# Kernel tuning notes

Measured on AMD Instinct MI355X. Metric: run time of the kernel, lower is better.

The kernel has to match this reference:

```python
import jax, jax.numpy as jnp
import numpy as np

BN_EPS = 1e-5


def setup_inputs() -> dict:
    key = jax.random.key(0)
    ks = jax.random.split(key, 8)
    B, C_IN, C_OUT, N, K = 4, 32, 64, 32768, 16
    feature = jax.random.normal(ks[0], (B, C_IN, N), dtype=jnp.float32)
    knn_inds = jax.random.randint(ks[1], (B, N, K), 0, N, dtype=jnp.int64)
    W1 = jax.random.normal(ks[2], (C_OUT, C_IN), dtype=jnp.float32) * 0.05
    W2 = jax.random.normal(ks[3], (C_OUT, C_IN), dtype=jnp.float32) * 0.05
    bn_gamma = jax.random.uniform(ks[4], (2 * C_OUT,), dtype=jnp.float32) + 0.5
    bn_beta = jax.random.normal(ks[5], (2 * C_OUT,), dtype=jnp.float32) * 0.1
    bn_mean = jax.random.normal(ks[6], (2 * C_OUT,), dtype=jnp.float32) * 0.1
    bn_var = jax.random.uniform(ks[7], (2 * C_OUT,), dtype=jnp.float32) + 0.5
    return {"feature": feature, "knn_inds": knn_inds, "W1": W1, "W2": W2,
            "bn_gamma": bn_gamma, "bn_beta": bn_beta, "bn_mean": bn_mean, "bn_var": bn_var}


def reference(feature, knn_inds, W1, W2, bn_gamma, bn_beta, bn_mean, bn_var):
    B, C_in, N = feature.shape
    K = knn_inds.shape[2]
    # 1x1 Conv1d == per-point GEMM
    local = jnp.einsum('oc,bcn->bon', W1, feature)   # (B, C_out, N)
    edge = jnp.einsum('oc,bcn->bon', W2, feature)    # (B, C_out, N)
    C = local.shape[1]
    # KNN gather: neighbour[b,c,n,j] = edge[b,c,knn_inds[b,n,j]]
    idx = knn_inds.reshape(B, 1, N * K)              # broadcast over channel dim
    neighbour = jnp.take_along_axis(edge, idx, axis=2).reshape(B, C, N, K)
    central = local[:, :, :, None]                   # (B, C, N, 1)
    diff = neighbour - central
    ef = jnp.concatenate([jnp.broadcast_to(central, (B, C, N, K)), diff], axis=1)  # (B, 2C, N, K)
    # BatchNorm2d (eval mode: running stats) + ReLU
    inv = (bn_gamma / jnp.sqrt(bn_var + BN_EPS)).reshape(1, 2 * C, 1, 1)
    shift = (bn_beta - bn_mean * bn_gamma / jnp.sqrt(bn_var + BN_EPS)).reshape(1, 2 * C, 1, 1)
    ef = jax.nn.relu(ef * inv + shift)
    return jnp.mean(ef, axis=3)                      # (B, 2C, N)
```

## Files before the change

### kernel.cpp

```cpp
#include <hip/hip_runtime.h>
#include <hip/hip_fp16.h>

#define CIN 32
#define COUT 64
#define NB 4
#define NPTS 32768
#define KNN 16

typedef unsigned short u16;
typedef unsigned char u8;
typedef float f2v __attribute__((ext_vector_type(2)));

__device__ __forceinline__ u16 f2h(float f) {
  _Float16 h = (_Float16)f;
  u16 u; __builtin_memcpy(&u, &h, 2); return u;
}
__device__ __forceinline__ f2v h2_to_f2(unsigned int u) {
  _Float16 a, b;
  __builtin_memcpy(&a, (const char*)&u, 2);
  __builtin_memcpy(&b, ((const char*)&u) + 2, 2);
  return (f2v){(float)a, (float)b};
}

__global__ __launch_bounds__(256) void k1_gemm(
    const float* __restrict__ feat, const float* __restrict__ W1,
    const float* __restrict__ W2, const float* __restrict__ gamma,
    const float* __restrict__ beta, const float* __restrict__ mean,
    const float* __restrict__ var, u16* __restrict__ lt, u8* __restrict__ et,
    float* __restrict__ out) {
  const int bid = blockIdx.x;
  const int b = bid >> 9;
  const int n0 = (bid & 511) << 6;
  const int t = threadIdx.x;
  const int lane = t & 63;
  const int wchunk = __builtin_amdgcn_readfirstlane(t >> 6);
  const int n = n0 + lane;

  f2v fv[16];
  const float* fp = feat + (size_t)b * CIN * NPTS + n;
#pragma unroll
  for (int c2 = 0; c2 < 16; ++c2)
    fv[c2] = (f2v){fp[(size_t)(2 * c2) * NPTS], fp[(size_t)(2 * c2 + 1) * NPTS]};

  const int half = wchunk >> 1;
  const int rbase = (wchunk & 1) * 32;
  const float* Wp = half ? W2 : W1;

  unsigned int pkh[16];
  unsigned int pk8[8];

#pragma unroll
  for (int oo = 0; oo < 32; oo += 4) {
    const float* w0 = Wp + (size_t)(rbase + oo) * CIN;
    const f2v* wr0 = reinterpret_cast<const f2v*>(w0);
    const f2v* wr1 = reinterpret_cast<const f2v*>(w0 + CIN);
    const f2v* wr2 = reinterpret_cast<const f2v*>(w0 + 2 * CIN);
    const f2v* wr3 = reinterpret_cast<const f2v*>(w0 + 3 * CIN);
    f2v p0 = (f2v)0.f, p1 = (f2v)0.f, p2 = (f2v)0.f, p3 = (f2v)0.f;
#pragma unroll
    for (int c2 = 0; c2 < 16; ++c2) {
      const f2v fc = fv[c2];
      p0 = __builtin_elementwise_fma(wr0[c2], fc, p0);
      p1 = __builtin_elementwise_fma(wr1[c2], fc, p1);
      p2 = __builtin_elementwise_fma(wr2[c2], fc, p2);
      p3 = __builtin_elementwise_fma(wr3[c2], fc, p3);
    }
    const float a0 = p0.x + p0.y, a1 = p1.x + p1.y;
    const float a2 = p2.x + p2.y, a3 = p3.x + p3.y;
    if (half == 0) {
      pkh[oo / 2]     = (unsigned)f2h(a0) | ((unsigned)f2h(a1) << 16);
      pkh[oo / 2 + 1] = (unsigned)f2h(a2) | ((unsigned)f2h(a3) << 16);
      const float acc[4] = {a0, a1, a2, a3};
#pragma unroll
      for (int i = 0; i < 4; ++i) {
        const int r = rbase + oo + i;
        const float iv = gamma[r] * rsqrtf(var[r] + 1e-5f);
        const float sh = beta[r] - mean[r] * iv;
        out[((size_t)b * 128 + r) * NPTS + n] = fmaxf(fmaf(acc[i], iv, sh), 0.f);
      }
    } else {
      int u = 0;
      u = __builtin_amdgcn_cvt_pk_fp8_f32(a0, a1, u, false);
      u = __builtin_amdgcn_cvt_pk_fp8_f32(a2, a3, u, true);
      pk8[oo / 4] = (unsigned)u;
    }
  }
  if (half == 0) {
    uint4* dp = reinterpret_cast<uint4*>(lt + ((size_t)(b * NPTS + n)) * COUT + rbase);
#pragma unroll
    for (int q = 0; q < 4; ++q)
      dp[q] = make_uint4(pkh[4 * q], pkh[4 * q + 1], pkh[4 * q + 2], pkh[4 * q + 3]);
  } else {
    uint4* dp = reinterpret_cast<uint4*>(et + ((size_t)(b * NPTS + n)) * COUT + rbase);
    dp[0] = make_uint4(pk8[0], pk8[1], pk8[2], pk8[3]);
    dp[1] = make_uint4(pk8[4], pk8[5], pk8[6], pk8[7]);
  }
}

__global__ __launch_bounds__(256) void k2_gather(
    const u16* __restrict__ lt, const u8* __restrict__ et,
    const int* __restrict__ knn, const float* __restrict__ gamma,
    const float* __restrict__ beta, const float* __restrict__ mean,
    const float* __restrict__ var, float* __restrict__ out) {
  __shared__ float obuf[64 * 33];
  int bid = blockIdx.x;
  bid = (bid & 7) * 512 + (bid >> 3);
  const int b = bid >> 10;
  const int n_blk = (bid & 1023) << 5;
  const int t = threadIdx.x;
  const int w = t >> 6;
  const int lane = t & 63;
  const int nn = lane >> 3;
  const int cg = lane & 7;
  const int ch = cg * 8;

  f2v inv[4], sh[4];
#pragma unroll
  for (int i = 0; i < 4; ++i) {
    const int r0 = 64 + ch + 2 * i;
    const float iv0 = gamma[r0] * rsqrtf(var[r0] + 1e-5f);
    const float iv1 = gamma[r0 + 1] * rsqrtf(var[r0 + 1] + 1e-5f);
    inv[i] = (f2v){iv0, iv1};
    sh[i] = (f2v){beta[r0] - mean[r0] * iv0, beta[r0 + 1] - mean[r0 + 1] * iv1};
  }

  const int n = n_blk + w * 8 + nn;
  const size_t rowbase = (size_t)b * NPTS;

  const int4* kp = reinterpret_cast<const int4*>(knn + (rowbase + n) * KNN);
  const int4 kv0 = kp[0], kv1 = kp[1], kv2 = kp[2], kv3 = kp[3];
  const uint4 lv = *reinterpret_cast<const uint4*>(lt + (rowbase + n) * COUT + ch);

  const u8* etb = et + rowbase * COUT + ch;
  uint2 e[16];
  const int idx[16] = {kv0.x, kv0.y, kv0.z, kv0.w, kv1.x, kv1.y, kv1.z, kv1.w,
                       kv2.x, kv2.y, kv2.z, kv2.w, kv3.x, kv3.y, kv3.z, kv3.w};
#pragma unroll
  for (int k = 0; k < 16; ++k)
    e[k] = *reinterpret_cast<const uint2*>(etb + ((size_t)idx[k] << 6));

  const unsigned int* lu = reinterpret_cast<const unsigned int*>(&lv);
  f2v tt[4];
#pragma unroll
  for (int i = 0; i < 4; ++i) tt[i] = sh[i] - h2_to_f2(lu[i]) * inv[i];

  f2v acc[4] = {(f2v)0.f, (f2v)0.f, (f2v)0.f, (f2v)0.f};
  const f2v zero = (f2v)0.f;
#pragma unroll
  for (int k = 0; k < 16; ++k) {
    const f2v d0 = __builtin_amdgcn_cvt_pk_f32_fp8(e[k].x, false);
    const f2v d1 = __builtin_amdgcn_cvt_pk_f32_fp8(e[k].x, true);
    const f2v d2 = __builtin_amdgcn_cvt_pk_f32_fp8(e[k].y, false);
    const f2v d3 = __builtin_amdgcn_cvt_pk_f32_fp8(e[k].y, true);
    acc[0] += __builtin_elementwise_max(__builtin_elementwise_fma(d0, inv[0], tt[0]), zero);
    acc[1] += __builtin_elementwise_max(__builtin_elementwise_fma(d1, inv[1], tt[1]), zero);
    acc[2] += __builtin_elementwise_max(__builtin_elementwise_fma(d2, inv[2], tt[2]), zero);
    acc[3] += __builtin_elementwise_max(__builtin_elementwise_fma(d3, inv[3], tt[3]), zero);
  }

  const int ncol = w * 8 + nn;
#pragma unroll
  for (int i = 0; i < 4; ++i) {
    obuf[(ch + 2 * i) * 33 + ncol] = acc[i].x * 0.0625f;
    obuf[(ch + 2 * i + 1) * 33 + ncol] = acc[i].y * 0.0625f;
  }
  __syncthreads();
#pragma unroll
  for (int r = 0; r < 2; ++r) {
    const int c = (t >> 3) + (r << 5);
    const int nn4 = (t & 7) * 4;
    float4 v = make_float4(obuf[c * 33 + nn4], obuf[c * 33 + nn4 + 1],
                           obuf[c * 33 + nn4 + 2], obuf[c * 33 + nn4 + 3]);
    *reinterpret_cast<float4*>(out + ((size_t)b * 128 + 64 + c) * NPTS + n_blk + nn4) = v;
  }
}

extern "C" void kernel_launch(void* const* d_in, const int* in_sizes, int n_in,
                              void* d_out, int out_size, void* d_ws, size_t ws_size,
                              hipStream_t stream) {
  const float* feat  = (const float*)d_in[0];
  const int*   knn   = (const int*)d_in[1];
  const float* W1    = (const float*)d_in[2];
  const float* W2    = (const float*)d_in[3];
  const float* gamma = (const float*)d_in[4];
  const float* beta  = (const float*)d_in[5];
  const float* mean  = (const float*)d_in[6];
  const float* var   = (const float*)d_in[7];
  float* out = (float*)d_out;

  u16* lt = (u16*)d_ws;
  u8* et = (u8*)(lt + (size_t)NB * NPTS * COUT);

  k1_gemm<<<dim3(NB * NPTS / 64), 256, 0, stream>>>(feat, W1, W2, gamma, beta,
                                                    mean, var, lt, et, out);
  k2_gather<<<dim3(NB * NPTS / 32), 256, 0, stream>>>(lt, et, knn, gamma, beta,
                                                      mean, var, out);
}
```

Before: 55.07 us.

## Move central-channel output into gather kernel and add nontemporal loads/stores

The first 64 output channels (BN+ReLU of the local conv) are now computed in the gather kernel from the fp16 local tensor it already loads, instead of being written by the GEMM kernel with strided per-channel stores. The gather kernel stages all 128 channels in a larger shared tile and writes them with coalesced float4 stores. Nontemporal hints are added to streaming loads and stores (features, knn indices, local tensor, output) to keep the cache free for the randomly gathered edge tensor. The central output is now derived from fp16-rounded values rather than fp32, which adds a little error, and the larger shared buffer may lower occupancy.

```diff
diff --git a/kernel.cpp b/kernel.cpp
--- a/kernel.cpp
+++ b/kernel.cpp
@@ -10,6 +10,10 @@
 typedef unsigned short u16;
 typedef unsigned char u8;
 typedef float f2v __attribute__((ext_vector_type(2)));
+typedef float f4v __attribute__((ext_vector_type(4)));
+typedef int i4v __attribute__((ext_vector_type(4)));
+typedef unsigned int u4v __attribute__((ext_vector_type(4)));
+typedef unsigned int u2v __attribute__((ext_vector_type(2)));
 
 __device__ __forceinline__ u16 f2h(float f) {
   _Float16 h = (_Float16)f;
@@ -24,10 +28,7 @@
 
 __global__ __launch_bounds__(256) void k1_gemm(
     const float* __restrict__ feat, const float* __restrict__ W1,
-    const float* __restrict__ W2, const float* __restrict__ gamma,
-    const float* __restrict__ beta, const float* __restrict__ mean,
-    const float* __restrict__ var, u16* __restrict__ lt, u8* __restrict__ et,
-    float* __restrict__ out) {
+    const float* __restrict__ W2, u16* __restrict__ lt, u8* __restrict__ et) {
   const int bid = blockIdx.x;
   const int b = bid >> 9;
   const int n0 = (bid & 511) << 6;
@@ -40,7 +41,8 @@
   const float* fp = feat + (size_t)b * CIN * NPTS + n;
 #pragma unroll
   for (int c2 = 0; c2 < 16; ++c2)
-    fv[c2] = (f2v){fp[(size_t)(2 * c2) * NPTS], fp[(size_t)(2 * c2 + 1) * NPTS]};
+    fv[c2] = (f2v){__builtin_nontemporal_load(fp + (size_t)(2 * c2) * NPTS),
+                   __builtin_nontemporal_load(fp + (size_t)(2 * c2 + 1) * NPTS)};
 
   const int half = wchunk >> 1;
   const int rbase = (wchunk & 1) * 32;
@@ -70,14 +72,6 @@
     if (half == 0) {
       pkh[oo / 2]     = (unsigned)f2h(a0) | ((unsigned)f2h(a1) << 16);
       pkh[oo / 2 + 1] = (unsigned)f2h(a2) | ((unsigned)f2h(a3) << 16);
-      const float acc[4] = {a0, a1, a2, a3};
-#pragma unroll
-      for (int i = 0; i < 4; ++i) {
-        const int r = rbase + oo + i;
-        const float iv = gamma[r] * rsqrtf(var[r] + 1e-5f);
-        const float sh = beta[r] - mean[r] * iv;
-        out[((size_t)b * 128 + r) * NPTS + n] = fmaxf(fmaf(acc[i], iv, sh), 0.f);
-      }
     } else {
       int u = 0;
       u = __builtin_amdgcn_cvt_pk_fp8_f32(a0, a1, u, false);
@@ -86,14 +80,16 @@
     }
   }
   if (half == 0) {
-    uint4* dp = reinterpret_cast<uint4*>(lt + ((size_t)(b * NPTS + n)) * COUT + rbase);
-#pragma unroll
-    for (int q = 0; q < 4; ++q)
-      dp[q] = make_uint4(pkh[4 * q], pkh[4 * q + 1], pkh[4 * q + 2], pkh[4 * q + 3]);
+    u4v* dp = reinterpret_cast<u4v*>(lt + ((size_t)(b * NPTS + n)) * COUT + rbase);
+#pragma unroll
+    for (int q = 0; q < 4; ++q) {
+      const u4v v = {pkh[4 * q], pkh[4 * q + 1], pkh[4 * q + 2], pkh[4 * q + 3]};
+      __builtin_nontemporal_store(v, dp + q);
+    }
   } else {
-    uint4* dp = reinterpret_cast<uint4*>(et + ((size_t)(b * NPTS + n)) * COUT + rbase);
-    dp[0] = make_uint4(pk8[0], pk8[1], pk8[2], pk8[3]);
-    dp[1] = make_uint4(pk8[4], pk8[5], pk8[6], pk8[7]);
+    u4v* dp = reinterpret_cast<u4v*>(et + ((size_t)(b * NPTS + n)) * COUT + rbase);
+    dp[0] = (u4v){pk8[0], pk8[1], pk8[2], pk8[3]};
+    dp[1] = (u4v){pk8[4], pk8[5], pk8[6], pk8[7]};
   }
 }
 
@@ -102,7 +98,7 @@
     const int* __restrict__ knn, const float* __restrict__ gamma,
     const float* __restrict__ beta, const float* __restrict__ mean,
     const float* __restrict__ var, float* __restrict__ out) {
-  __shared__ float obuf[64 * 33];
+  __shared__ float obuf[128 * 33];
   int bid = blockIdx.x;
   bid = (bid & 7) * 512 + (bid >> 3);
   const int b = bid >> 10;
@@ -114,35 +110,53 @@
   const int cg = lane & 7;
   const int ch = cg * 8;
 
-  f2v inv[4], sh[4];
-#pragma unroll
-  for (int i = 0; i < 4; ++i) {
-    const int r0 = 64 + ch + 2 * i;
-    const float iv0 = gamma[r0] * rsqrtf(var[r0] + 1e-5f);
-    const float iv1 = gamma[r0 + 1] * rsqrtf(var[r0 + 1] + 1e-5f);
-    inv[i] = (f2v){iv0, iv1};
-    sh[i] = (f2v){beta[r0] - mean[r0] * iv0, beta[r0 + 1] - mean[r0 + 1] * iv1};
-  }
-
   const int n = n_blk + w * 8 + nn;
+  const int col = w * 8 + nn;
   const size_t rowbase = (size_t)b * NPTS;
 
-  const int4* kp = reinterpret_cast<const int4*>(knn + (rowbase + n) * KNN);
-  const int4 kv0 = kp[0], kv1 = kp[1], kv2 = kp[2], kv3 = kp[3];
-  const uint4 lv = *reinterpret_cast<const uint4*>(lt + (rowbase + n) * COUT + ch);
+  const i4v* kp = reinterpret_cast<const i4v*>(knn + (rowbase + n) * KNN);
+  const i4v kv0 = __builtin_nontemporal_load(kp);
+  const i4v kv1 = __builtin_nontemporal_load(kp + 1);
+  const i4v kv2 = __builtin_nontemporal_load(kp + 2);
+  const i4v kv3 = __builtin_nontemporal_load(kp + 3);
+  const u4v lv = __builtin_nontemporal_load(
+      reinterpret_cast<const u4v*>(lt + (rowbase + n) * COUT + ch));
 
   const u8* etb = et + rowbase * COUT + ch;
-  uint2 e[16];
   const int idx[16] = {kv0.x, kv0.y, kv0.z, kv0.w, kv1.x, kv1.y, kv1.z, kv1.w,
                        kv2.x, kv2.y, kv2.z, kv2.w, kv3.x, kv3.y, kv3.z, kv3.w};
+  u2v e[16];
 #pragma unroll
   for (int k = 0; k < 16; ++k)
-    e[k] = *reinterpret_cast<const uint2*>(etb + ((size_t)idx[k] << 6));
-
-  const unsigned int* lu = reinterpret_cast<const unsigned int*>(&lv);
-  f2v tt[4];
-#pragma unroll
-  for (int i = 0; i < 4; ++i) tt[i] = sh[i] - h2_to_f2(lu[i]) * inv[i];
+    e[k] = *reinterpret_cast<const u2v*>(etb + ((size_t)idx[k] << 6));
+
+  const unsigned int lw[4] = {lv.x, lv.y, lv.z, lv.w};
+  f2v inv2[4], tt[4];
+#pragma unroll
+  for (int i = 0; i < 4; ++i) {
+    const f2v l = h2_to_f2(lw[i]);
+    {
+      const int r0 = ch + 2 * i;
+      const float iv0 = gamma[r0] * rsqrtf(var[r0] + 1e-5f);
+      const float iv1 = gamma[r0 + 1] * rsqrtf(var[r0 + 1] + 1e-5f);
+      const f2v iv = (f2v){iv0, iv1};
+      const f2v sh = (f2v){beta[r0] - mean[r0] * iv0,
+                           beta[r0 + 1] - mean[r0 + 1] * iv1};
+      const f2v cen = __builtin_elementwise_max(
+          __builtin_elementwise_fma(l, iv, sh), (f2v)0.f);
+      obuf[(ch + 2 * i) * 33 + col] = cen.x;
+      obuf[(ch + 2 * i + 1) * 33 + col] = cen.y;
+    }
+    {
+      const int r0 = 64 + ch + 2 * i;
+      const float iv0 = gamma[r0] * rsqrtf(var[r0] + 1e-5f);
+      const float iv1 = gamma[r0 + 1] * rsqrtf(var[r0 + 1] + 1e-5f);
+      inv2[i] = (f2v){iv0, iv1};
+      const f2v sh = (f2v){beta[r0] - mean[r0] * iv0,
+                           beta[r0 + 1] - mean[r0 + 1] * iv1};
+      tt[i] = sh - l * inv2[i];
+    }
+  }
 
   f2v acc[4] = {(f2v)0.f, (f2v)0.f, (f2v)0.f, (f2v)0.f};
   const f2v zero = (f2v)0.f;
@@ -152,26 +166,25 @@
     const f2v d1 = __builtin_amdgcn_cvt_pk_f32_fp8(e[k].x, true);
     const f2v d2 = __builtin_amdgcn_cvt_pk_f32_fp8(e[k].y, false);
     const f2v d3 = __builtin_amdgcn_cvt_pk_f32_fp8(e[k].y, true);
-    acc[0] += __builtin_elementwise_max(__builtin_elementwise_fma(d0, inv[0], tt[0]), zero);
-    acc[1] += __builtin_elementwise_max(__builtin_elementwise_fma(d1, inv[1], tt[1]), zero);
-    acc[2] += __builtin_elementwise_max(__builtin_elementwise_fma(d2, inv[2], tt[2]), zero);
-    acc[3] += __builtin_elementwise_max(__builtin_elementwise_fma(d3, inv[3], tt[3]), zero);
-  }
-
-  const int ncol = w * 8 + nn;
+    acc[0] += __builtin_elementwise_max(__builtin_elementwise_fma(d0, inv2[0], tt[0]), zero);
+    acc[1] += __builtin_elementwise_max(__builtin_elementwise_fma(d1, inv2[1], tt[1]), zero);
+    acc[2] += __builtin_elementwise_max(__builtin_elementwise_fma(d2, inv2[2], tt[2]), zero);
+    acc[3] += __builtin_elementwise_max(__builtin_elementwise_fma(d3, inv2[3], tt[3]), zero);
+  }
 #pragma unroll
   for (int i = 0; i < 4; ++i) {
-    obuf[(ch + 2 * i) * 33 + ncol] = acc[i].x * 0.0625f;
-    obuf[(ch + 2 * i + 1) * 33 + ncol] = acc[i].y * 0.0625f;
+    obuf[(64 + ch + 2 * i) * 33 + col] = acc[i].x * 0.0625f;
+    obuf[(64 + ch + 2 * i + 1) * 33 + col] = acc[i].y * 0.0625f;
   }
   __syncthreads();
 #pragma unroll
-  for (int r = 0; r < 2; ++r) {
-    const int c = (t >> 3) + (r << 5);
+  for (int r = 0; r < 4; ++r) {
+    const int c = r * 32 + (t >> 3);
     const int nn4 = (t & 7) * 4;
-    float4 v = make_float4(obuf[c * 33 + nn4], obuf[c * 33 + nn4 + 1],
-                           obuf[c * 33 + nn4 + 2], obuf[c * 33 + nn4 + 3]);
-    *reinterpret_cast<float4*>(out + ((size_t)b * 128 + 64 + c) * NPTS + n_blk + nn4) = v;
+    const f4v v = {obuf[c * 33 + nn4], obuf[c * 33 + nn4 + 1],
+                   obuf[c * 33 + nn4 + 2], obuf[c * 33 + nn4 + 3]};
+    __builtin_nontemporal_store(
+        v, reinterpret_cast<f4v*>(out + ((size_t)b * 128 + c) * NPTS + n_blk + nn4));
   }
 }
 
@@ -191,8 +204,7 @@
   u16* lt = (u16*)d_ws;
   u8* et = (u8*)(lt + (size_t)NB * NPTS * COUT);
 
-  k1_gemm<<<dim3(NB * NPTS / 64), 256, 0, stream>>>(feat, W1, W2, gamma, beta,
-                                                    mean, var, lt, et, out);
+  k1_gemm<<<dim3(NB * NPTS / 64), 256, 0, stream>>>(feat, W1, W2, lt, et);
   k2_gather<<<dim3(NB * NPTS / 32), 256, 0, stream>>>(lt, et, knn, gamma, beta,
                                                       mean, var, out);
 }
```

Measured after the change: 75.42 us. 37.0% more time.
